# Kernel tuning notes

Hardware: AMD Instinct MI355X
Metric: run time of the kernel (lower is better)

The kernel has to match this reference:

```python
import jax, jax.numpy as jnp
import numpy as np


def setup_inputs() -> dict:
    key = jax.random.key(0)
    k1, k2, k3 = jax.random.split(key, 3)
    B, C, D, S = 16, 80, 1024, 14  # batch, num_classes, feature dim, conv size
    return {
        "batch_size": B,
        "img_feature_map": jax.random.normal(k1, (B, D, S, S), dtype=jnp.float32),
        "word_features": jax.random.normal(k2, (C, D), dtype=jnp.float32),
        "fc_a_w": jax.random.normal(k3, (D,), dtype=jnp.float32) / np.float32(np.sqrt(D)),
        "fc_a_b": jnp.zeros((), dtype=jnp.float32),
    }


def reference(batch_size, img_feature_map, word_features, fc_a_w, fc_a_b):
    # img_feature_map: [B, D, H, W] -> [B, H, W, D]
    img = jnp.transpose(img_feature_map, (0, 2, 3, 1))
    # class-wise gated feature: tanh(img * word) -> [B, H, W, C, D]
    gated = jnp.tanh(img[:, :, :, None, :] * word_features[None, None, None, :, :])
    # rank-1 linear score: [B, H, W, C]
    scores = jnp.einsum('bhwcd,d->bhwc', gated, fc_a_w) + fc_a_b
    B, H, W, C = scores.shape
    # softmax over spatial positions (H*W) per (batch, class)
    coef = jax.nn.softmax(scores.reshape(B, H * W, C), axis=1).reshape(B, H, W, C)
    # attention-weighted spatial pooling -> [B, C, D]
    return jnp.einsum('bhwc,bhwd->bcd', coef, img)
```

## Files before the change

kernel.cpp:

```cpp
#include <hip/hip_runtime.h>

#define BB 16
#define CC 80
#define DD 1024
#define HW 196
#define NSP (BB * HW)
#define NCH 8
#define DCH 128
#define CPB 4
#define NCQ (CC / CPB)
#define PTC 16
#define TWO_LOG2E 2.8853900817779268f

__global__ __launch_bounds__(256) void scores_k(const float* __restrict__ img,
                                                const float* __restrict__ word,
                                                const float* __restrict__ fa,
                                                float* __restrict__ partial,
                                                float* __restrict__ imgT) {
    const int g = blockIdx.x * 256 + threadIdx.x;
    if (g >= NSP) return;
    const int b  = g / HW;
    const int hw = g - b * HW;
    const int d0 = blockIdx.y * DCH;
    const int c0 = blockIdx.z * CPB;

    const float* ip = img + ((size_t)b * DD + d0) * HW + hw;

    float p[CPB];
#pragma unroll
    for (int k = 0; k < CPB; ++k) p[k] = 0.f;

    for (int q = 0; q < DCH / 32; ++q) {
        float iv[32];
        const float* qp = ip + (size_t)q * 32 * HW;
#pragma unroll
        for (int i = 0; i < 32; ++i)
            iv[i] = qp[(size_t)i * HW];

        if (blockIdx.z == 0) {
            float4* tp = (float4*)(imgT + (size_t)g * DD + d0 + q * 32);
#pragma unroll
            for (int i = 0; i < 8; ++i)
                tp[i] = make_float4(iv[4 * i], iv[4 * i + 1], iv[4 * i + 2], iv[4 * i + 3]);
        }

#pragma unroll
        for (int i = 0; i < 32; ++i)
            iv[i] *= TWO_LOG2E;

        const float* fp = fa + d0 + q * 32;
#pragma unroll
        for (int k = 0; k < CPB; ++k) {
            const float* wp = word + (size_t)(c0 + k) * DD + d0 + q * 32;
            float p0 = 0.f, p1 = 0.f;
#pragma unroll
            for (int i = 0; i < 32; i += 2) {
                float y0 = iv[i]     * wp[i];
                float y1 = iv[i + 1] * wp[i + 1];
                float e0 = __builtin_amdgcn_exp2f(y0);
                float e1 = __builtin_amdgcn_exp2f(y1);
                float r0 = __builtin_amdgcn_rcpf(e0 + 1.f);
                float r1 = __builtin_amdgcn_rcpf(e1 + 1.f);
                p0 = fmaf(fp[i],     r0, p0);
                p1 = fmaf(fp[i + 1], r1, p1);
            }
            p[k] += p0 + p1;
        }
    }

#pragma unroll
    for (int k = 0; k < CPB; ++k)
        partial[(((size_t)b * NCH + blockIdx.y) * CC + (c0 + k)) * HW + hw]
            = (-TWO_LOG2E) * p[k];
}

__global__ __launch_bounds__(256) void poolT_k(const float* __restrict__ imgT,
                                               const float* __restrict__ partial,
                                               float* __restrict__ out) {
    __shared__ float ct[PTC * HW];
    const int b   = blockIdx.x;
    const int dt0 = blockIdx.y * 256;
    const int cg  = blockIdx.z * PTC;
    const int t   = threadIdx.x;
    const int w   = t >> 6, l = t & 63;

#pragma unroll
    for (int rr = 0; rr < 4; ++rr) {
        const int r = 4 * w + rr;
        const int c = cg + r;
        float x0 = 0.f, x1 = 0.f, x2 = 0.f, x3 = 0.f;
#pragma unroll
        for (int ch = 0; ch < NCH; ++ch) {
            const float* pp = partial + (((size_t)b * NCH + ch) * CC + c) * HW;
            x0 += pp[l];
            x1 += pp[l + 64];
            x2 += pp[l + 128];
            if (l < HW - 192) x3 += pp[l + 192];
        }
        float x3m = (l < HW - 192) ? x3 : -3.4e38f;

        float m = fmaxf(fmaxf(x0, x1), fmaxf(x2, x3m));
#pragma unroll
        for (int off = 32; off >= 1; off >>= 1) m = fmaxf(m, __shfl_xor(m, off, 64));

        float e0 = __builtin_amdgcn_exp2f(x0 - m);
        float e1 = __builtin_amdgcn_exp2f(x1 - m);
        float e2 = __builtin_amdgcn_exp2f(x2 - m);
        float e3 = (l < HW - 192) ? __builtin_amdgcn_exp2f(x3 - m) : 0.f;

        float s = (e0 + e1) + (e2 + e3);
#pragma unroll
        for (int off = 32; off >= 1; off >>= 1) s += __shfl_xor(s, off, 64);

        float inv = __builtin_amdgcn_rcpf(s);
        float* cr = ct + r * HW;
        cr[l]       = e0 * inv;
        cr[l + 64]  = e1 * inv;
        cr[l + 128] = e2 * inv;
        if (l < HW - 192) cr[l + 192] = e3 * inv;
    }
    __syncthreads();

    const float* crow = ct + (4 * w) * HW;
    const float* ib = imgT + ((size_t)b * HW) * DD + dt0 + 4 * l;

    float4 acc0 = {0,0,0,0}, acc1 = {0,0,0,0}, acc2 = {0,0,0,0}, acc3 = {0,0,0,0};
    for (int h = 0; h < HW; h += 4) {
        float4 i0 = *(const float4*)(ib + (size_t)(h    ) * DD);
        float4 i1 = *(const float4*)(ib + (size_t)(h + 1) * DD);
        float4 i2 = *(const float4*)(ib + (size_t)(h + 2) * DD);
        float4 i3 = *(const float4*)(ib + (size_t)(h + 3) * DD);
        float4 c0v = *(const float4*)(crow + h);
        float4 c1v = *(const float4*)(crow + HW + h);
        float4 c2v = *(const float4*)(crow + 2 * HW + h);
        float4 c3v = *(const float4*)(crow + 3 * HW + h);
#define ACC4(A, CV)                                                      \
        A.x = fmaf(CV.x, i0.x, fmaf(CV.y, i1.x, fmaf(CV.z, i2.x, fmaf(CV.w, i3.x, A.x)))); \
        A.y = fmaf(CV.x, i0.y, fmaf(CV.y, i1.y, fmaf(CV.z, i2.y, fmaf(CV.w, i3.y, A.y)))); \
        A.z = fmaf(CV.x, i0.z, fmaf(CV.y, i1.z, fmaf(CV.z, i2.z, fmaf(CV.w, i3.z, A.z)))); \
        A.w = fmaf(CV.x, i0.w, fmaf(CV.y, i1.w, fmaf(CV.z, i2.w, fmaf(CV.w, i3.w, A.w))));
        ACC4(acc0, c0v)
        ACC4(acc1, c1v)
        ACC4(acc2, c2v)
        ACC4(acc3, c3v)
#undef ACC4
    }

    float* ob = out + ((size_t)b * CC + cg + 4 * w) * DD + dt0 + 4 * l;
    *(float4*)(ob)              = acc0;
    *(float4*)(ob + DD)         = acc1;
    *(float4*)(ob + 2 * (size_t)DD) = acc2;
    *(float4*)(ob + 3 * (size_t)DD) = acc3;
}

extern "C" void kernel_launch(void* const* d_in, const int* in_sizes, int n_in,
                              void* d_out, int out_size, void* d_ws, size_t ws_size,
                              hipStream_t stream) {
    const float* img  = (const float*)d_in[1];
    const float* word = (const float*)d_in[2];
    const float* fa   = (const float*)d_in[3];
    float* out = (float*)d_out;

    float* partial = (float*)d_ws;
    float* imgT    = partial + (size_t)BB * NCH * CC * HW;

    scores_k<<<dim3((NSP + 255) / 256, NCH, NCQ), 256, 0, stream>>>(img, word, fa, partial, imgT);
    poolT_k<<<dim3(BB, DD / 256, CC / PTC), 256, 0, stream>>>(imgT, partial, out);
}
```

Before: 174.6 us.

## Restructure pooling kernel to compute four classes per block with scalar d per thread

The pooling kernel now computes 4 classes per block instead of 16, and each thread handles a single d column with scalar loads instead of a float4 of 4 d columns. The grid grows from 5 to 20 class groups, giving 4x more blocks. The aim is more parallelism and occupancy with less work per thread. In exchange, imgT is re-read from global or L2 four times as often, once per class group rather than once per 16 classes, and the softmax over the partials runs per 4-class block.

```diff
diff --git a/kernel.cpp b/kernel.cpp
--- a/kernel.cpp
+++ b/kernel.cpp
@@ -9,7 +9,6 @@
 #define DCH 128
 #define CPB 4
 #define NCQ (CC / CPB)
-#define PTC 16
 #define TWO_LOG2E 2.8853900817779268f
 
 __global__ __launch_bounds__(256) void scores_k(const float* __restrict__ img,
@@ -74,20 +73,18 @@
             = (-TWO_LOG2E) * p[k];
 }
 
-__global__ __launch_bounds__(256) void poolT_k(const float* __restrict__ imgT,
+__global__ __launch_bounds__(256) void pool2_k(const float* __restrict__ imgT,
                                                const float* __restrict__ partial,
                                                float* __restrict__ out) {
-    __shared__ float ct[PTC * HW];
+    __shared__ float ct[4 * HW];
     const int b   = blockIdx.x;
     const int dt0 = blockIdx.y * 256;
-    const int cg  = blockIdx.z * PTC;
+    const int cg  = blockIdx.z * 4;
     const int t   = threadIdx.x;
     const int w   = t >> 6, l = t & 63;
 
-#pragma unroll
-    for (int rr = 0; rr < 4; ++rr) {
-        const int r = 4 * w + rr;
-        const int c = cg + r;
+    {
+        const int c = cg + w;
         float x0 = 0.f, x1 = 0.f, x2 = 0.f, x3 = 0.f;
 #pragma unroll
         for (int ch = 0; ch < NCH; ++ch) {
@@ -113,7 +110,7 @@
         for (int off = 32; off >= 1; off >>= 1) s += __shfl_xor(s, off, 64);
 
         float inv = __builtin_amdgcn_rcpf(s);
-        float* cr = ct + r * HW;
+        float* cr = ct + w * HW;
         cr[l]       = e0 * inv;
         cr[l + 64]  = e1 * inv;
         cr[l + 128] = e2 * inv;
@@ -121,36 +118,30 @@
     }
     __syncthreads();
 
-    const float* crow = ct + (4 * w) * HW;
-    const float* ib = imgT + ((size_t)b * HW) * DD + dt0 + 4 * l;
+    const float* ib = imgT + (size_t)b * HW * DD + dt0 + t;
 
-    float4 acc0 = {0,0,0,0}, acc1 = {0,0,0,0}, acc2 = {0,0,0,0}, acc3 = {0,0,0,0};
+    float a0 = 0.f, a1 = 0.f, a2 = 0.f, a3 = 0.f;
+#pragma unroll 7
     for (int h = 0; h < HW; h += 4) {
-        float4 i0 = *(const float4*)(ib + (size_t)(h    ) * DD);
-        float4 i1 = *(const float4*)(ib + (size_t)(h + 1) * DD);
-        float4 i2 = *(const float4*)(ib + (size_t)(h + 2) * DD);
-        float4 i3 = *(const float4*)(ib + (size_t)(h + 3) * DD);
-        float4 c0v = *(const float4*)(crow + h);
-        float4 c1v = *(const float4*)(crow + HW + h);
-        float4 c2v = *(const float4*)(crow + 2 * HW + h);
-        float4 c3v = *(const float4*)(crow + 3 * HW + h);
-#define ACC4(A, CV)                                                      \
-        A.x = fmaf(CV.x, i0.x, fmaf(CV.y, i1.x, fmaf(CV.z, i2.x, fmaf(CV.w, i3.x, A.x)))); \
-        A.y = fmaf(CV.x, i0.y, fmaf(CV.y, i1.y, fmaf(CV.z, i2.y, fmaf(CV.w, i3.y, A.y)))); \
-        A.z = fmaf(CV.x, i0.z, fmaf(CV.y, i1.z, fmaf(CV.z, i2.z, fmaf(CV.w, i3.z, A.z)))); \
-        A.w = fmaf(CV.x, i0.w, fmaf(CV.y, i1.w, fmaf(CV.z, i2.w, fmaf(CV.w, i3.w, A.w))));
-        ACC4(acc0, c0v)
-        ACC4(acc1, c1v)
-        ACC4(acc2, c2v)
-        ACC4(acc3, c3v)
-#undef ACC4
+        float i0 = ib[(size_t)(h    ) * DD];
+        float i1 = ib[(size_t)(h + 1) * DD];
+        float i2 = ib[(size_t)(h + 2) * DD];
+        float i3 = ib[(size_t)(h + 3) * DD];
+        float4 c0v = *(const float4*)(ct + h);
+        float4 c1v = *(const float4*)(ct + HW + h);
+        float4 c2v = *(const float4*)(ct + 2 * HW + h);
+        float4 c3v = *(const float4*)(ct + 3 * HW + h);
+        a0 = fmaf(c0v.x, i0, fmaf(c0v.y, i1, fmaf(c0v.z, i2, fmaf(c0v.w, i3, a0))));
+        a1 = fmaf(c1v.x, i0, fmaf(c1v.y, i1, fmaf(c1v.z, i2, fmaf(c1v.w, i3, a1))));
+        a2 = fmaf(c2v.x, i0, fmaf(c2v.y, i1, fmaf(c2v.z, i2, fmaf(c2v.w, i3, a2))));
+        a3 = fmaf(c3v.x, i0, fmaf(c3v.y, i1, fmaf(c3v.z, i2, fmaf(c3v.w, i3, a3))));
     }
 
-    float* ob = out + ((size_t)b * CC + cg + 4 * w) * DD + dt0 + 4 * l;
-    *(float4*)(ob)              = acc0;
-    *(float4*)(ob + DD)         = acc1;
-    *(float4*)(ob + 2 * (size_t)DD) = acc2;
-    *(float4*)(ob + 3 * (size_t)DD) = acc3;
+    float* ob = out + ((size_t)b * CC + cg) * DD + dt0 + t;
+    ob[0]              = a0;
+    ob[DD]             = a1;
+    ob[2 * (size_t)DD] = a2;
+    ob[3 * (size_t)DD] = a3;
 }
 
 extern "C" void kernel_launch(void* const* d_in, const int* in_sizes, int n_in,
@@ -165,5 +156,5 @@
     float* imgT    = partial + (size_t)BB * NCH * CC * HW;
 
     scores_k<<<dim3((NSP + 255) / 256, NCH, NCQ), 256, 0, stream>>>(img, word, fa, partial, imgT);
-    poolT_k<<<dim3(BB, DD / 256, CC / PTC), 256, 0, stream>>>(imgT, partial, out);
+    pool2_k<<<dim3(BB, DD / 256, CC / 4), 256, 0, stream>>>(imgT, partial, out);
 }
```

Result: faster. 150.9 us (-13.6%).
